# Kernel tuning notes

Measured on AMD Instinct MI355X. Metric: run time of the kernel, lower is better.

Reference implementation:

```python
import jax, jax.numpy as jnp
import numpy as np

H, W_FREQ, DIM = 16, 9, 768

def setup_inputs() -> dict:
    key = jax.random.key(0)
    k1, k2 = jax.random.split(key)
    x = jax.random.normal(k1, (256, 256, 768), dtype=jnp.float32)
    complex_weight = jax.random.normal(k2, (H, W_FREQ, DIM, 2), dtype=jnp.float32) * 0.02
    return {"x": x, "complex_weight": complex_weight}

def reference(x, complex_weight):
    B, N, C = x.shape  # N=256, C=768
    xg = x.reshape(B, 16, 16, 768)
    # 2D orthonormal rFFT over the 16x16 token grid -> (B, 16, 9, 768) complex
    xf = jnp.fft.rfftn(xg, axes=(1, 2), norm="ortho")
    weight = complex_weight[..., 0] + 1j * complex_weight[..., 1]  # (16, 9, 768)
    xf = xf * weight
    out = jnp.fft.irfftn(xf, s=(16, 16), axes=(1, 2), norm="ortho")
    return out.reshape(B, N, C)
```

## Files before the change

kernel.cpp:

```cpp
#include <hip/hip_runtime.h>


#define DIM 768
#define CT 32
#define NCT (DIM / CT)
#define NB 256
#define IP 258

#define R2c  0.70710678118654752f
#define C1c  0.92387953251128674f
#define S1cc 0.38268343236508978f
#define INV512  (1.f / 512.f)
#define INV256  (1.f / 256.f)
#define INV1024 (1.f / 1024.f)

template <int SGN>
__device__ __forceinline__ void fft16(float* xr, float* xi) {
#define SWP(a, b) { float t_ = xr[a]; xr[a] = xr[b]; xr[b] = t_; t_ = xi[a]; xi[a] = xi[b]; xi[b] = t_; }
  SWP(1, 8) SWP(2, 4) SWP(3, 12) SWP(5, 10) SWP(7, 14) SWP(11, 13)
#undef SWP
#define BF1(a, b) { float tr = xr[b], ti = xi[b]; xr[b] = xr[a] - tr; xi[b] = xi[a] - ti; xr[a] += tr; xi[a] += ti; }
#define BFI(a, b) { float tr, ti; if (SGN < 0) { tr = xi[b]; ti = -xr[b]; } else { tr = -xi[b]; ti = xr[b]; } \
                    xr[b] = xr[a] - tr; xi[b] = xi[a] - ti; xr[a] += tr; xi[a] += ti; }
#define BFW(a, b, Wr, Wi) { float tr = (Wr) * xr[b] - (Wi) * xi[b], ti = (Wr) * xi[b] + (Wi) * xr[b]; \
                            xr[b] = xr[a] - tr; xi[b] = xi[a] - ti; xr[a] += tr; xi[a] += ti; }
  BF1(0, 1) BF1(2, 3) BF1(4, 5) BF1(6, 7) BF1(8, 9) BF1(10, 11) BF1(12, 13) BF1(14, 15)
  BF1(0, 2) BF1(4, 6) BF1(8, 10) BF1(12, 14)
  BFI(1, 3) BFI(5, 7) BFI(9, 11) BFI(13, 15)
  BF1(0, 4) BF1(8, 12)
  BFW(1, 5, R2c, SGN * R2c) BFW(9, 13, R2c, SGN * R2c)
  BFI(2, 6) BFI(10, 14)
  BFW(3, 7, -R2c, SGN * R2c) BFW(11, 15, -R2c, SGN * R2c)
  BF1(0, 8)
  BFW(1, 9, C1c, SGN * S1cc)
  BFW(2, 10, R2c, SGN * R2c)
  BFW(3, 11, S1cc, SGN * C1c)
  BFI(4, 12)
  BFW(5, 13, -S1cc, SGN * C1c)
  BFW(6, 14, -R2c, SGN * R2c)
  BFW(7, 15, -C1c, SGN * S1cc)
#undef BF1
#undef BFI
#undef BFW
}

__global__ __launch_bounds__(256, 4) void gf2_kernel(const float* __restrict__ x,
                                                     const float* __restrict__ w,
                                                     float* __restrict__ out) {
  __shared__ __align__(16) float2 E[16 * IP];
  float4* E4 = (float4*)E;

  const int blk = blockIdx.x;
  const int ct = blk >> 8;
  const int b  = blk & 255;
  const int c0 = ct * CT;
  const int t  = threadIdx.x;
  const int r  = t >> 4;
  const int p  = t & 15;

  {
    const float2* xp = (const float2*)(x + (size_t)b * 196608 + (size_t)r * 12288 + c0) + p;
    float zr[16], zi[16];
#pragma unroll
    for (int j = 0; j < 16; j++) { float2 v = xp[j * 384]; zr[j] = v.x; zi[j] = v.y; }
    fft16<-1>(zr, zi);
    E4[r * 129 + p] = make_float4(zr[0], zr[8], zi[0], zi[8]);
#pragma unroll
    for (int k = 1; k <= 7; k++) {
      const int m = 16 - k;
      float Ar = zr[k] + zr[m], Ai = zi[k] - zi[m];
      float Br = zi[k] + zi[m], Bi = zr[m] - zr[k];
      E4[r * 129 + k * 16 + p] = make_float4(Ar, Ai, Br, Bi);
    }
  }
  __syncthreads();

  {
    const int s = t >> 5;
    const int c = t & 31;
    float gr[16], gi[16];
    const float2* col = E + s * 32 + c;
#pragma unroll
    for (int i = 0; i < 16; i++) { float2 v = col[i * IP]; gr[i] = v.x; gi[i] = v.y; }
    __syncthreads();

    if (s == 0) {
      fft16<-1>(gr, gi);
      const float* wc = w + (size_t)(c0 + c) * 2;
      {
        float2 a0 = *(const float2*)(wc);
        float2 a8 = *(const float2*)(wc + 12288);
        float2 b0 = *(const float2*)(wc + 8 * 13824);
        float2 b8 = *(const float2*)(wc + 8 * 13824 + 12288);
        gr[0] = gr[0] * (a0.x * INV256);
        gi[0] = gi[0] * (a8.x * INV256);
        gr[8] = gr[8] * (b0.x * INV256);
        gi[8] = gi[8] * (b8.x * INV256);
      }
#pragma unroll
      for (int k = 1; k <= 7; k++) {
        const int m = 16 - k;
        float2 a0 = *(const float2*)(wc + (size_t)k * 13824);
        float2 m0 = *(const float2*)(wc + (size_t)m * 13824);
        float2 a8 = *(const float2*)(wc + (size_t)k * 13824 + 12288);
        float2 m8 = *(const float2*)(wc + (size_t)m * 13824 + 12288);
        float Vpr = (a0.x + m0.x + a8.x + m8.x) * INV1024;
        float Vpi = (a0.y - m0.y + a8.y - m8.y) * INV1024;
        float Vmr = (a0.x + m0.x - a8.x - m8.x) * INV1024;
        float Vmi = (a0.y - m0.y - a8.y + m8.y) * INV1024;
        float ur = gr[k], ui = gi[k], vr = gr[m], vi = gi[m];
        float nkr = ur * Vpr - ui * Vpi + vr * Vmr + vi * Vmi;
        float nki = ur * Vpi + ui * Vpr + vr * Vmi - vi * Vmr;
        float nmr = vr * Vpr + vi * Vpi + ur * Vmr - ui * Vmi;
        float nmi = vi * Vpr - vr * Vpi - ur * Vmi - ui * Vmr;
        gr[k] = nkr; gi[k] = nki; gr[m] = nmr; gi[m] = nmi;
      }
      fft16<1>(gr, gi);
    } else {
      float wvr[16], wvi[16];
      const float* wp = w + (size_t)(s * 768 + c0 + c) * 2;
#pragma unroll
      for (int k1 = 0; k1 < 16; k1++) {
        float2 wv = *(const float2*)(wp + (size_t)k1 * 13824);
        wvr[k1] = wv.x * INV512; wvi[k1] = wv.y * INV512;
      }
      fft16<-1>(gr, gi);
#pragma unroll
      for (int k1 = 0; k1 < 16; k1++) {
        float yr = gr[k1] * wvr[k1] - gi[k1] * wvi[k1];
        float yi = gr[k1] * wvi[k1] + gi[k1] * wvr[k1];
        gr[k1] = yr; gi[k1] = yi;
      }
      fft16<1>(gr, gi);
    }

    float2* colo = E + s * 32 + c;
#pragma unroll
    for (int n1 = 0; n1 < 16; n1++) { colo[n1 * IP] = make_float2(gr[n1], gi[n1]); }
  }
  __syncthreads();

  {
    float hr[16], hi[16];
#pragma unroll
    for (int k = 0; k <= 7; k++) {
      float4 v = E4[r * 129 + k * 16 + p];
      if (k == 0) {
        hr[0] = v.x; hi[0] = v.z;
        hr[8] = v.y; hi[8] = v.w;
      } else {
        hr[k] = v.x - v.w;      hi[k] = v.y + v.z;
        hr[16 - k] = v.x + v.w; hi[16 - k] = v.z - v.y;
      }
    }
    fft16<1>(hr, hi);
    float2* op = (float2*)(out + (size_t)b * 196608 + (size_t)r * 12288 + c0) + p;
#pragma unroll
    for (int n2 = 0; n2 < 16; n2++) { op[n2 * 384] = make_float2(hr[n2], hi[n2]); }
  }
}

extern "C" void kernel_launch(void* const* d_in, const int* in_sizes, int n_in,
                              void* d_out, int out_size, void* d_ws, size_t ws_size,
                              hipStream_t stream) {
  const float* x = (const float*)d_in[0];
  const float* w = (const float*)d_in[1];
  float* out = (float*)d_out;
  dim3 grid(NCT * NB);
  dim3 block(256);
  hipLaunchKernelGGL(gf2_kernel, grid, block, 0, stream, x, w, out);
}
```

Before: 102.5 us.

## Process two batch tiles per block with upfront loads and lighter LDS barriers

```diff
diff --git a/kernel.cpp b/kernel.cpp
--- a/kernel.cpp
+++ b/kernel.cpp
@@ -4,7 +4,6 @@
 #define DIM 768
 #define CT 32
 #define NCT (DIM / CT)
-#define NB 256
 #define IP 258
 
 #define R2c  0.70710678118654752f
@@ -13,6 +12,8 @@
 #define INV512  (1.f / 512.f)
 #define INV256  (1.f / 256.f)
 #define INV1024 (1.f / 1024.f)
+
+#define BARL() { asm volatile("s_waitcnt lgkmcnt(0)" ::: "memory"); __builtin_amdgcn_s_barrier(); }
 
 template <int SGN>
 __device__ __forceinline__ void fft16(float* xr, float* xi) {
@@ -44,120 +45,129 @@
 #undef BFW
 }
 
-__global__ __launch_bounds__(256, 4) void gf2_kernel(const float* __restrict__ x,
+__global__ __launch_bounds__(256, 4) void gf9_kernel(const float* __restrict__ x,
                                                      const float* __restrict__ w,
                                                      float* __restrict__ out) {
   __shared__ __align__(16) float2 E[16 * IP];
   float4* E4 = (float4*)E;
 
   const int blk = blockIdx.x;
-  const int ct = blk >> 8;
-  const int b  = blk & 255;
+  const int ct = blk >> 7;
+  const int bp = blk & 127;
+  const int b0 = bp * 2;
   const int c0 = ct * CT;
   const int t  = threadIdx.x;
   const int r  = t >> 4;
   const int p  = t & 15;
+  const int s  = t >> 5;
+  const int c  = t & 31;
 
+  float zr0[16], zi0[16], zr1[16], zi1[16];
   {
-    const float2* xp = (const float2*)(x + (size_t)b * 196608 + (size_t)r * 12288 + c0) + p;
-    float zr[16], zi[16];
+    const float2* xp = (const float2*)(x + (size_t)b0 * 196608 + (size_t)r * 12288 + c0) + p;
 #pragma unroll
-    for (int j = 0; j < 16; j++) { float2 v = xp[j * 384]; zr[j] = v.x; zi[j] = v.y; }
-    fft16<-1>(zr, zi);
-    E4[r * 129 + p] = make_float4(zr[0], zr[8], zi[0], zi[8]);
+    for (int j = 0; j < 16; j++) { float2 v = xp[j * 384]; zr0[j] = v.x; zi0[j] = v.y; }
+    const float2* xq = xp + 98304;
 #pragma unroll
-    for (int k = 1; k <= 7; k++) {
-      const int m = 16 - k;
-      float Ar = zr[k] + zr[m], Ai = zi[k] - zi[m];
-      float Br = zi[k] + zi[m], Bi = zr[m] - zr[k];
-      E4[r * 129 + k * 16 + p] = make_float4(Ar, Ai, Br, Bi);
-    }
+    for (int j = 0; j < 16; j++) { float2 v = xq[j * 384]; zr1[j] = v.x; zi1[j] = v.y; }
   }
-  __syncthreads();
 
-  {
-    const int s = t >> 5;
-    const int c = t & 31;
-    float gr[16], gi[16];
-    const float2* col = E + s * 32 + c;
-#pragma unroll
-    for (int i = 0; i < 16; i++) { float2 v = col[i * IP]; gr[i] = v.x; gi[i] = v.y; }
-    __syncthreads();
+#define TILE_BODY(ZR, ZI, BB)                                                  \
+  {                                                                            \
+               \
+    fft16<-1>(ZR, ZI);                                                         \
+    {                                                                          \
+      E4[r * 129 + p] = make_float4(ZR[0], ZR[8], ZI[0], ZI[8]);               \
+    }                                                                          \
+    _Pragma("unroll")                                                          \
+    for (int k = 1; k <= 7; k++) {                                             \
+      const int m = 16 - k;                                                    \
+      float Ar = ZR[k] + ZR[m], Ai = ZI[k] - ZI[m];                            \
+      float Br = ZI[k] + ZI[m], Bi = ZR[m] - ZR[k];                            \
+      E4[r * 129 + k * 16 + p] = make_float4(Ar, Ai, Br, Bi);                  \
+    }                                                                          \
+    BARL();                                                                    \
+                                     \
+    {                                                                          \
+      float gr[16], gi[16];                                                    \
+      const float2* col = E + s * 32 + c;                                      \
+      _Pragma("unroll")                                                        \
+      for (int i = 0; i < 16; i++) { float2 v = col[i * IP]; gr[i] = v.x; gi[i] = v.y; } \
+      BARL();                           \
+      fft16<-1>(gr, gi);                                                       \
+      if (s == 0) {                                                            \
+        const float* wc = w + (size_t)(c0 + c) * 2;                            \
+        {                                                                      \
+          float2 a0 = *(const float2*)(wc);                                    \
+          float2 a8 = *(const float2*)(wc + 12288);                            \
+          float2 b0_ = *(const float2*)(wc + 8 * 13824);                       \
+          float2 b8 = *(const float2*)(wc + 8 * 13824 + 12288);                \
+          gr[0] = gr[0] * (a0.x * INV256);                                     \
+          gi[0] = gi[0] * (a8.x * INV256);                                     \
+          gr[8] = gr[8] * (b0_.x * INV256);                                    \
+          gi[8] = gi[8] * (b8.x * INV256);                                     \
+        }                                                                      \
+        _Pragma("unroll")                                                      \
+        for (int k = 1; k <= 7; k++) {                                         \
+          const int m = 16 - k;                                                \
+          float2 a0 = *(const float2*)(wc + (size_t)k * 13824);                \
+          float2 m0 = *(const float2*)(wc + (size_t)m * 13824);                \
+          float2 a8 = *(const float2*)(wc + (size_t)k * 13824 + 12288);        \
+          float2 m8 = *(const float2*)(wc + (size_t)m * 13824 + 12288);        \
+          float Vpr = (a0.x + m0.x + a8.x + m8.x) * INV1024;                   \
+          float Vpi = (a0.y - m0.y + a8.y - m8.y) * INV1024;                   \
+          float Vmr = (a0.x + m0.x - a8.x - m8.x) * INV1024;                   \
+          float Vmi = (a0.y - m0.y - a8.y + m8.y) * INV1024;                   \
+          float ur = gr[k], ui = gi[k], vr = gr[m], vi = gi[m];                \
+          float nkr = ur * Vpr - ui * Vpi + vr * Vmr + vi * Vmi;               \
+          float nki = ur * Vpi + ui * Vpr + vr * Vmi - vi * Vmr;               \
+          float nmr = vr * Vpr + vi * Vpi + ur * Vmr - ui * Vmi;               \
+          float nmi = vi * Vpr - vr * Vpi - ur * Vmi - ui * Vmr;               \
+          gr[k] = nkr; gi[k] = nki; gr[m] = nmr; gi[m] = nmi;                  \
+        }                                                                      \
+      } else {                                                                 \
+        const float* wp = w + (size_t)(s * 768 + c0 + c) * 2;                  \
+        _Pragma("unroll")                                                      \
+        for (int k1 = 0; k1 < 16; k1++) {                                      \
+          float2 wv = *(const float2*)(wp + (size_t)k1 * 13824);               \
+          const float wr_ = wv.x * INV512, wi_ = wv.y * INV512;                \
+          float yr = gr[k1] * wr_ - gi[k1] * wi_;                              \
+          float yi = gr[k1] * wi_ + gi[k1] * wr_;                              \
+          gr[k1] = yr; gi[k1] = yi;                                            \
+        }                                                                      \
+      }                                                                        \
+      fft16<1>(gr, gi);                                                        \
+      float2* colo = E + s * 32 + c;                                           \
+      _Pragma("unroll")                                                        \
+      for (int n1 = 0; n1 < 16; n1++) { colo[n1 * IP] = make_float2(gr[n1], gi[n1]); } \
+    }                                                                          \
+    BARL();                                                                    \
+                              \
+    {                                                                          \
+      float hr[16], hq[16];                                                    \
+      _Pragma("unroll")                                                        \
+      for (int k = 0; k <= 7; k++) {                                           \
+        float4 v = E4[r * 129 + k * 16 + p];                                   \
+        if (k == 0) {                                                          \
+          hr[0] = v.x; hq[0] = v.z;                                            \
+          hr[8] = v.y; hq[8] = v.w;                                            \
+        } else {                                                               \
+          hr[k] = v.x - v.w;      hq[k] = v.y + v.z;                           \
+          hr[16 - k] = v.x + v.w; hq[16 - k] = v.z - v.y;                      \
+        }                                                                      \
+      }                                                                        \
+      fft16<1>(hr, hq);                                                        \
+      float2* op = (float2*)(out + (size_t)(BB) * 196608 + (size_t)r * 12288 + c0) + p; \
+      _Pragma("unroll")                                                        \
+      for (int n2 = 0; n2 < 16; n2++) { op[n2 * 384] = make_float2(hr[n2], hq[n2]); } \
+    }                                                                          \
+  }
 
-    if (s == 0) {
-      fft16<-1>(gr, gi);
-      const float* wc = w + (size_t)(c0 + c) * 2;
-      {
-        float2 a0 = *(const float2*)(wc);
-        float2 a8 = *(const float2*)(wc + 12288);
-        float2 b0 = *(const float2*)(wc + 8 * 13824);
-        float2 b8 = *(const float2*)(wc + 8 * 13824 + 12288);
-        gr[0] = gr[0] * (a0.x * INV256);
-        gi[0] = gi[0] * (a8.x * INV256);
-        gr[8] = gr[8] * (b0.x * INV256);
-        gi[8] = gi[8] * (b8.x * INV256);
-      }
-#pragma unroll
-      for (int k = 1; k <= 7; k++) {
-        const int m = 16 - k;
-        float2 a0 = *(const float2*)(wc + (size_t)k * 13824);
-        float2 m0 = *(const float2*)(wc + (size_t)m * 13824);
-        float2 a8 = *(const float2*)(wc + (size_t)k * 13824 + 12288);
-        float2 m8 = *(const float2*)(wc + (size_t)m * 13824 + 12288);
-        float Vpr = (a0.x + m0.x + a8.x + m8.x) * INV1024;
-        float Vpi = (a0.y - m0.y + a8.y - m8.y) * INV1024;
-        float Vmr = (a0.x + m0.x - a8.x - m8.x) * INV1024;
-        float Vmi = (a0.y - m0.y - a8.y + m8.y) * INV1024;
-        float ur = gr[k], ui = gi[k], vr = gr[m], vi = gi[m];
-        float nkr = ur * Vpr - ui * Vpi + vr * Vmr + vi * Vmi;
-        float nki = ur * Vpi + ui * Vpr + vr * Vmi - vi * Vmr;
-        float nmr = vr * Vpr + vi * Vpi + ur * Vmr - ui * Vmi;
-        float nmi = vi * Vpr - vr * Vpi - ur * Vmi - ui * Vmr;
-        gr[k] = nkr; gi[k] = nki; gr[m] = nmr; gi[m] = nmi;
-      }
-      fft16<1>(gr, gi);
-    } else {
-      float wvr[16], wvi[16];
-      const float* wp = w + (size_t)(s * 768 + c0 + c) * 2;
-#pragma unroll
-      for (int k1 = 0; k1 < 16; k1++) {
-        float2 wv = *(const float2*)(wp + (size_t)k1 * 13824);
-        wvr[k1] = wv.x * INV512; wvi[k1] = wv.y * INV512;
-      }
-      fft16<-1>(gr, gi);
-#pragma unroll
-      for (int k1 = 0; k1 < 16; k1++) {
-        float yr = gr[k1] * wvr[k1] - gi[k1] * wvi[k1];
-        float yi = gr[k1] * wvi[k1] + gi[k1] * wvr[k1];
-        gr[k1] = yr; gi[k1] = yi;
-      }
-      fft16<1>(gr, gi);
-    }
+  TILE_BODY(zr0, zi0, b0)
+  BARL();
+  TILE_BODY(zr1, zi1, b0 + 1)
 
-    float2* colo = E + s * 32 + c;
-#pragma unroll
-    for (int n1 = 0; n1 < 16; n1++) { colo[n1 * IP] = make_float2(gr[n1], gi[n1]); }
-  }
-  __syncthreads();
-
-  {
-    float hr[16], hi[16];
-#pragma unroll
-    for (int k = 0; k <= 7; k++) {
-      float4 v = E4[r * 129 + k * 16 + p];
-      if (k == 0) {
-        hr[0] = v.x; hi[0] = v.z;
-        hr[8] = v.y; hi[8] = v.w;
-      } else {
-        hr[k] = v.x - v.w;      hi[k] = v.y + v.z;
-        hr[16 - k] = v.x + v.w; hi[16 - k] = v.z - v.y;
-      }
-    }
-    fft16<1>(hr, hi);
-    float2* op = (float2*)(out + (size_t)b * 196608 + (size_t)r * 12288 + c0) + p;
-#pragma unroll
-    for (int n2 = 0; n2 < 16; n2++) { op[n2 * 384] = make_float2(hr[n2], hi[n2]); }
-  }
+#undef TILE_BODY
 }
 
 extern "C" void kernel_launch(void* const* d_in, const int* in_sizes, int n_in,
@@ -166,7 +176,7 @@
   const float* x = (const float*)d_in[0];
   const float* w = (const float*)d_in[1];
   float* out = (float*)d_out;
-  dim3 grid(NCT * NB);
+  dim3 grid(NCT * 128);
   dim3 block(256);
-  hipLaunchKernelGGL(gf2_kernel, grid, block, 0, stream, x, w, out);
+  hipLaunchKernelGGL(gf9_kernel, grid, block, 0, stream, x, w, out);
 }
```

Result: slower. 121.9 us (+19.0%).
